# Kernel tuning notes

Measured on AMD Instinct MI355X. Metric: run time of the kernel, lower is better.

Reference implementation:

```python
import jax, jax.numpy as jnp
import numpy as np

B, S_IMG, S_TXT, P, D, HEADS, HD = 1, 2048, 512, 4, 3072, 24, 128


def rmsnorm(x, weight=None, eps=1e-6):
    var = jnp.mean(jnp.square(x), axis=-1, keepdims=True)
    y = x * jax.lax.rsqrt(var + eps)
    return y * weight if weight is not None else y


def apply_rope(x, cos, sin):
    # x: [B,H,S,Dh]; cos/sin: [S,Dh]; interleaved real/imag rotation (diffusers use_real_unbind_dim=-1)
    xr = x.reshape(*x.shape[:-1], -1, 2)
    rot = jnp.stack([-xr[..., 1], xr[..., 0]], axis=-1).reshape(x.shape)
    return x * cos[None, None] + rot * sin[None, None]


def sdpa(q, k, v):
    scores = jnp.einsum('bhqd,bhkd->bhqk', q, k) / jnp.sqrt(jnp.asarray(q.shape[-1], q.dtype))
    return jnp.einsum('bhqk,bhkd->bhqd', jax.nn.softmax(scores, axis=-1), v)


def heads_split(x):
    # [B,S,D] -> [B,H,S,Dh]
    return x.reshape(x.shape[0], x.shape[1], HEADS, HD).transpose(0, 2, 1, 3)


def heads_merge(x):
    # [B,H,S,Dh] -> [B,S,D]
    return x.transpose(0, 2, 1, 3).reshape(x.shape[0], x.shape[2], HEADS * HD)


def setup_inputs() -> dict:
    key = jax.random.key(0)
    ks = jax.random.split(key, 32)
    init = lambda k, shape: (jax.random.normal(k, shape, dtype=jnp.float32) * 0.02)
    inp = {
        'hidden_states': jax.random.normal(ks[0], (B, S_IMG, D), dtype=jnp.float32),
        'encoder_hidden_states': jax.random.normal(ks[1], (B, S_TXT, D), dtype=jnp.float32),
        'ip_encoder_hidden_states': jax.random.normal(ks[2], (B, P, D), dtype=jnp.float32),
        'layer_scale': jax.random.uniform(ks[3], (B,), dtype=jnp.float32),
        'Wq': init(ks[4], (D, D)), 'bq': jnp.zeros((D,), jnp.float32),
        'Wk': init(ks[5], (D, D)), 'bk': jnp.zeros((D,), jnp.float32),
        'Wv': init(ks[6], (D, D)), 'bv': jnp.zeros((D,), jnp.float32),
        'norm_q_w': jnp.ones((HD,), jnp.float32),
        'norm_k_w': jnp.ones((HD,), jnp.float32),
        'Waq': init(ks[7], (D, D)), 'baq': jnp.zeros((D,), jnp.float32),
        'Wak': init(ks[8], (D, D)), 'bak': jnp.zeros((D,), jnp.float32),
        'Wav': init(ks[9], (D, D)), 'bav': jnp.zeros((D,), jnp.float32),
        'norm_aq_w': jnp.ones((HD,), jnp.float32),
        'norm_ak_w': jnp.ones((HD,), jnp.float32),
        'Wk_ip': init(ks[10], (D, D)),
        'Wv_ip': init(ks[11], (D, D)),
        'Wo': init(ks[12], (D, D)), 'bo': jnp.zeros((D,), jnp.float32),
        'Wao': init(ks[13], (D, D)), 'bao': jnp.zeros((D,), jnp.float32),
    }
    # rotary cos/sin over the joint (text+image) sequence, interleaved freqs per diffusers FLUX
    pos = jnp.arange(S_TXT + S_IMG, dtype=jnp.float32)
    inv_freq = 1.0 / (10000.0 ** (jnp.arange(0, HD, 2, dtype=jnp.float32) / HD))
    angles = pos[:, None] * inv_freq[None, :]            # [S, HD/2]
    angles = jnp.repeat(angles, 2, axis=-1)              # [S, HD]
    inp['cos'] = jnp.cos(angles)
    inp['sin'] = jnp.sin(angles)
    return inp


IP_SCALE = 1.0  # self.scale


def reference(hidden_states, encoder_hidden_states, ip_encoder_hidden_states, cos, sin,
              layer_scale, Wq, bq, Wk, bk, Wv, bv, norm_q_w, norm_k_w,
              Waq, baq, Wak, bak, Wav, bav, norm_aq_w, norm_ak_w,
              Wk_ip, Wv_ip, Wo, bo, Wao, bao):
    # image-stream projections
    q = heads_split(hidden_states @ Wq.T + bq)
    k = heads_split(hidden_states @ Wk.T + bk)
    v = heads_split(hidden_states @ Wv.T + bv)
    q = rmsnorm(q, norm_q_w, 1e-6)
    k = rmsnorm(k, norm_k_w, 1e-6)

    # IP-adapter cross-attention (queries = image tokens, kv = IP tokens)
    ip_k = rmsnorm(heads_split(ip_encoder_hidden_states @ Wk_ip.T), None, 1e-5)
    ip_v = heads_split(ip_encoder_hidden_states @ Wv_ip.T)
    ip_out = heads_merge(sdpa(q, ip_k, ip_v))            # [B, S_img, D]

    # text (encoder) stream projections, prepended to joint sequence
    eq = rmsnorm(heads_split(encoder_hidden_states @ Waq.T + baq), norm_aq_w, 1e-6)
    ek = rmsnorm(heads_split(encoder_hidden_states @ Wak.T + bak), norm_ak_w, 1e-6)
    ev = heads_split(encoder_hidden_states @ Wav.T + bav)
    q = jnp.concatenate([eq, q], axis=2)
    k = jnp.concatenate([ek, k], axis=2)
    v = jnp.concatenate([ev, v], axis=2)

    q = apply_rope(q, cos, sin)
    k = apply_rope(k, cos, sin)

    out = heads_merge(sdpa(q, k, v))                     # [B, S_txt+S_img, D]
    n_txt = encoder_hidden_states.shape[1]
    enc_out, img_out = out[:, :n_txt], out[:, n_txt:]

    ls = layer_scale.reshape(-1, 1, 1)
    img_out = img_out + IP_SCALE * ls * ip_out
    img_out = img_out @ Wo.T + bo
    enc_out = enc_out @ Wao.T + bao
    return (img_out, enc_out)
```

## Files before the change

kernel.cpp:

```cpp
#include <hip/hip_runtime.h>

typedef _Float16 half_t;
typedef _Float16 half2v __attribute__((ext_vector_type(2)));
typedef _Float16 half4v __attribute__((ext_vector_type(4)));
typedef _Float16 half8v __attribute__((ext_vector_type(8)));
typedef float    float4v __attribute__((ext_vector_type(4)));
typedef short    short8v __attribute__((ext_vector_type(8)));

#define S_IMG 2048
#define S_TXT 512
#define S_TOT 2560
#define NH    24
#define HD    128
#define DM    3072

__device__ __forceinline__ void gload16(const void* g, void* l) {
  __builtin_amdgcn_global_load_lds(
      (const __attribute__((address_space(1))) unsigned int*)g,
      (__attribute__((address_space(3))) unsigned int*)l, 16, 0, 0);
}

__global__ void cvt_act_kernel(const float* __restrict__ hs, const float* __restrict__ enc,
                               half_t* __restrict__ d) {
  const long NHS = (long)S_IMG * DM;
  const long TOT = NHS + (long)S_TXT * DM;
  long i = ((long)blockIdx.x * 256 + threadIdx.x) * 8;
  long stride = (long)gridDim.x * 256 * 8;
  for (; i < TOT; i += stride) {
    const float* s = i < NHS ? hs + i : enc + (i - NHS);
    float4v v0 = *(const float4v*)(s);
    float4v v1 = *(const float4v*)(s + 4);
    half8v h;
    h[0] = (half_t)v0[0]; h[1] = (half_t)v0[1]; h[2] = (half_t)v0[2]; h[3] = (half_t)v0[3];
    h[4] = (half_t)v1[0]; h[5] = (half_t)v1[1]; h[6] = (half_t)v1[2]; h[7] = (half_t)v1[3];
    *(half8v*)(d + i) = h;
  }
}

__global__ void cvt3_kernel(const float* __restrict__ s0, const float* __restrict__ s1,
                            const float* __restrict__ s2,
                            half_t* __restrict__ d0, half_t* __restrict__ d1,
                            half_t* __restrict__ d2, int n) {
  const float* s = blockIdx.y == 0 ? s0 : (blockIdx.y == 1 ? s1 : s2);
  half_t* d = blockIdx.y == 0 ? d0 : (blockIdx.y == 1 ? d1 : d2);
  int i = (blockIdx.x * 256 + threadIdx.x) * 8;
  int stride = gridDim.x * 256 * 8;
  for (; i < n; i += stride) {
    float4v v0 = *(const float4v*)(s + i);
    float4v v1 = *(const float4v*)(s + i + 4);
    half8v h;
    h[0] = (half_t)v0[0]; h[1] = (half_t)v0[1]; h[2] = (half_t)v0[2]; h[3] = (half_t)v0[3];
    h[4] = (half_t)v1[0]; h[5] = (half_t)v1[1]; h[6] = (half_t)v1[2]; h[7] = (half_t)v1[3];
    *(half8v*)(d + i) = h;
  }
}

template <typename OUT>
__device__ __forceinline__ void gemm_tile(half_t* As, half_t* Bs,
                                          const half_t* __restrict__ A,
                                          const half_t* __restrict__ Bt,
                                          const float* __restrict__ bias,
                                          OUT* __restrict__ C, int bm, int bn) {
  const int K = DM, N = DM;
  const int tid = threadIdx.x, wid = tid >> 6, l = tid & 63;
  const int wm = (wid >> 1) * 64, wn = (wid & 1) * 64;
  const int l15 = l & 15, l4 = l >> 4;
  float4v acc[4][4] = {};

  const int scol = ((l & 3) ^ ((l >> 3) & 3)) * 8;
  const half_t* ga = A + (long)(bm + wid * 32 + (l >> 2)) * K + scol;
  const half_t* gb = Bt + (long)(bn + wid * 32 + (l >> 2)) * K + scol;
  const long rowstep = 16l * K;

#define GSTAGE(T, SEL)                                                        \
  {                                                                           \
    char* a_d = (char*)As + (SEL) * 8192 + wid * 2048;                        \
    char* b_d = (char*)Bs + (SEL) * 8192 + wid * 2048;                        \
    int k0 = (T) * 32;                                                        \
    gload16(ga + k0, a_d);                                                    \
    gload16(ga + rowstep + k0, a_d + 1024);                                   \
    gload16(gb + k0, b_d);                                                    \
    gload16(gb + rowstep + k0, b_d + 1024);                                   \
  }

  GSTAGE(0, 0);
  GSTAGE(1, 1);

  const int NT = K / 32;
  const int cofs = (l4 * 16) ^ (((l15 >> 1) & 3) << 4);
  for (int t = 0; t < NT; t++) {
    int cur = t % 3;
    if (t + 1 < NT) asm volatile("s_waitcnt vmcnt(4)" ::: "memory");
    else            asm volatile("s_waitcnt vmcnt(0)" ::: "memory");
    __builtin_amdgcn_s_barrier();
    __builtin_amdgcn_sched_barrier(0);
    if (t + 2 < NT) GSTAGE(t + 2, (t + 2) % 3);
    __builtin_amdgcn_sched_barrier(0);
    const char* AsB = (const char*)As + cur * 8192;
    const char* BsB = (const char*)Bs + cur * 8192;
    half8v af[4], bf[4];
#pragma unroll
    for (int i = 0; i < 4; i++)
      af[i] = *(const half8v*)(AsB + (wm + i * 16 + l15) * 64 + cofs);
#pragma unroll
    for (int j = 0; j < 4; j++)
      bf[j] = *(const half8v*)(BsB + (wn + j * 16 + l15) * 64 + cofs);
    __builtin_amdgcn_s_setprio(1);
#pragma unroll
    for (int i = 0; i < 4; i++)
#pragma unroll
      for (int j = 0; j < 4; j++)
        acc[i][j] = __builtin_amdgcn_mfma_f32_16x16x32_f16(af[i], bf[j], acc[i][j], 0, 0, 0);
    __builtin_amdgcn_s_setprio(0);
  }
#undef GSTAGE
#pragma unroll
  for (int i = 0; i < 4; i++)
#pragma unroll
    for (int j = 0; j < 4; j++) {
      int row = bm + wm + i * 16 + l4 * 4;
      int col = bn + wn + j * 16 + l15;
      float bv = bias ? bias[col] : 0.0f;
#pragma unroll
      for (int r = 0; r < 4; r++) {
        float v = acc[i][j][r] + bv;
        C[(long)(row + r) * N + col] = (OUT)v;
      }
    }
}

template <int NROW>
__global__ __launch_bounds__(256) void gemm3_kernel(const half_t* __restrict__ A,
                                                    const half_t* __restrict__ W0,
                                                    const half_t* __restrict__ W1,
                                                    const half_t* __restrict__ W2,
                                                    const float* b0, const float* b1, const float* b2,
                                                    half_t* O0, half_t* O1, half_t* O2) {
  __shared__ half_t As[3 * 128 * 32];
  __shared__ half_t Bs[3 * 128 * 32];
  int b = blockIdx.x;
  int q = (72 * NROW) >> 3;
  int wg = (b & 7) * q + (b >> 3);
  int col = wg / NROW, row = wg % NROW;
  int sel = col / 24;
  const half_t* Bt = sel == 0 ? W0 : (sel == 1 ? W1 : W2);
  const float* bias = sel == 0 ? b0 : (sel == 1 ? b1 : b2);
  half_t* C = sel == 0 ? O0 : (sel == 1 ? O1 : O2);
  gemm_tile<half_t>(As, Bs, A, Bt, bias, C, row * 128, (col % 24) * 128);
}

__global__ __launch_bounds__(256) void gemm_out_kernel(const half_t* __restrict__ ocomb,
                                                       const half_t* __restrict__ Wo_h,
                                                       const half_t* __restrict__ Wao_h,
                                                       const float* bo, const float* bao,
                                                       float* out_img, float* out_enc) {
  __shared__ half_t As[3 * 128 * 32];
  __shared__ half_t Bs[3 * 128 * 32];
  int b = blockIdx.x;
  int wg = (b & 7) * 60 + (b >> 3);
  int col = wg / 20, r = wg % 20;
  bool enc = r >= 16;
  const half_t* A = enc ? ocomb : ocomb + (long)S_TXT * DM;
  int bm = (enc ? (r - 16) : r) * 128;
  gemm_tile<float>(As, Bs, A, enc ? Wao_h : Wo_h, enc ? bao : bo,
                   enc ? out_enc : out_img, bm, col * 128);
}

__global__ __launch_bounds__(256) void ip_proj_kernel(const float* __restrict__ x,
                                                      const float* __restrict__ Wk_ip,
                                                      const float* __restrict__ Wv_ip,
                                                      float* __restrict__ outk,
                                                      float* __restrict__ outv) {
  const float* W = blockIdx.y ? Wv_ip : Wk_ip;
  float* out = blockIdx.y ? outv : outk;
  int n = blockIdx.x * 4 + (threadIdx.x >> 6);
  int l = threadIdx.x & 63;
  const float* wr = W + (long)n * DM;
  float acc[4] = {0.f, 0.f, 0.f, 0.f};
  for (int k = l * 4; k < DM; k += 256) {
    float4v wv = *(const float4v*)(wr + k);
#pragma unroll
    for (int p = 0; p < 4; p++) {
      float4v xv = *(const float4v*)(x + p * DM + k);
      acc[p] += wv[0] * xv[0] + wv[1] * xv[1] + wv[2] * xv[2] + wv[3] * xv[3];
    }
  }
#pragma unroll
  for (int off = 32; off; off >>= 1)
#pragma unroll
    for (int p = 0; p < 4; p++) acc[p] += __shfl_xor(acc[p], off, 64);
  if (l == 0)
#pragma unroll
    for (int p = 0; p < 4; p++) out[p * DM + n] = acc[p];
}

__global__ void ip_norm_kernel(const float* __restrict__ kr, const float* __restrict__ vr,
                               half_t* __restrict__ kh, half_t* __restrict__ vh) {
  int t = blockIdx.x;
  int l = threadIdx.x;
  int d = l * 2;
  if (t < 96) {
    int base = (t / 24) * DM + (t % 24) * HD;
    float x0 = kr[base + d], x1 = kr[base + d + 1];
    float ss = x0 * x0 + x1 * x1;
#pragma unroll
    for (int off = 32; off; off >>= 1) ss += __shfl_xor(ss, off, 64);
    float r = rsqrtf(ss * (1.0f / HD) + 1e-5f);
    kh[base + d] = (half_t)(x0 * r);
    kh[base + d + 1] = (half_t)(x1 * r);
  } else {
    int t2 = t - 96;
    int base = (t2 / 24) * DM + (t2 % 24) * HD;
    vh[base + d] = (half_t)vr[base + d];
    vh[base + d + 1] = (half_t)vr[base + d + 1];
  }
}

__global__ __launch_bounds__(256) void prep_kernel(
    const half_t* __restrict__ qraw, const half_t* __restrict__ kraw,
    const half_t* __restrict__ eq, const half_t* __restrict__ ek,
    const float* __restrict__ nqw, const float* __restrict__ nkw,
    const float* __restrict__ naqw, const float* __restrict__ nakw,
    const float* __restrict__ cosb, const float* __restrict__ sinb,
    half_t* __restrict__ qcat, half_t* __restrict__ kcat, half_t* __restrict__ qnr) {
  int task = blockIdx.x * 4 + (threadIdx.x >> 6);
  int l = threadIdx.x & 63;
  int s = task / NH, h = task - (task / NH) * NH;
  int d = l * 2;
  const half_t *qs, *ks;
  const float *wq, *wk;
  if (s < S_TXT) {
    long base = (long)s * DM + h * HD;
    qs = eq + base; ks = ek + base;
    wq = naqw; wk = nakw;
  } else {
    long base = (long)(s - S_TXT) * DM + h * HD;
    qs = qraw + base; ks = kraw + base;
    wq = nqw; wk = nkw;
  }
  half2v qv = *(const half2v*)(qs + d);
  half2v kv = *(const half2v*)(ks + d);
  float q0 = (float)qv[0], q1 = (float)qv[1];
  float k0 = (float)kv[0], k1 = (float)kv[1];
  float ssq = q0 * q0 + q1 * q1;
  float ssk = k0 * k0 + k1 * k1;
#pragma unroll
  for (int off = 32; off; off >>= 1) {
    ssq += __shfl_xor(ssq, off, 64);
    ssk += __shfl_xor(ssk, off, 64);
  }
  float rq = rsqrtf(ssq * (1.0f / HD) + 1e-6f);
  float rk = rsqrtf(ssk * (1.0f / HD) + 1e-6f);
  float qn0 = q0 * rq * wq[d], qn1 = q1 * rq * wq[d + 1];
  float kn0 = k0 * rk * wk[d], kn1 = k1 * rk * wk[d + 1];
  if (s >= S_TXT) {
    half2v o; o[0] = (half_t)qn0; o[1] = (half_t)qn1;
    *(half2v*)(qnr + ((long)h * S_IMG + (s - S_TXT)) * HD + d) = o;
  }
  float c0 = cosb[s * HD + d], c1 = cosb[s * HD + d + 1];
  float s0 = sinb[s * HD + d], s1 = sinb[s * HD + d + 1];
  float qo0 = qn0 * c0 - qn1 * s0, qo1 = qn1 * c1 + qn0 * s1;
  float ko0 = kn0 * c0 - kn1 * s0, ko1 = kn1 * c1 + kn0 * s1;
  long ci = ((long)h * S_TOT + s) * HD + d;
  half2v oq; oq[0] = (half_t)qo0; oq[1] = (half_t)qo1;
  half2v ok; ok[0] = (half_t)ko0; ok[1] = (half_t)ko1;
  *(half2v*)(qcat + ci) = oq;
  *(half2v*)(kcat + ci) = ok;
}

__global__ __launch_bounds__(256) void vtrans_kernel(const half_t* __restrict__ ev,
                                                     const half_t* __restrict__ vraw,
                                                     half_t* __restrict__ vcatT) {
  __shared__ half_t T[64][136];
  int h = blockIdx.y, sb = blockIdx.x * 64;
  int t = threadIdx.x;
#pragma unroll
  for (int i = 0; i < 4; i++) {
    int c = t + i * 256;
    int row = c >> 4, col = (c & 15) * 8;
    int s = sb + row;
    const half_t* src = (s < S_TXT) ? ev + (long)s * DM + h * HD + col
                                    : vraw + (long)(s - S_TXT) * DM + h * HD + col;
    *(half8v*)&T[row][col] = *(const half8v*)src;
  }
  __syncthreads();
#pragma unroll
  for (int i = 0; i < 4; i++) {
    int c = t + i * 256;
    int d = c >> 3, sc = (c & 7) * 8;
    half8v v;
#pragma unroll
    for (int j = 0; j < 8; j++) v[j] = T[sc + j][d];
    *(half8v*)(vcatT + ((long)h * HD + d) * S_TOT + sb + sc) = v;
  }
}

__global__ __launch_bounds__(256) void ip_attn_kernel(const half_t* __restrict__ qnr,
                                                      const half_t* __restrict__ kh,
                                                      const half_t* __restrict__ vh,
                                                      half_t* __restrict__ ipout) {
  int tid = threadIdx.x;
  int task = blockIdx.x * 16 + (tid >> 4);
  int l16 = tid & 15;
  int h = task >> 11;
  int s = task & 2047;
  int d = l16 * 8;
  half8v qv = *(const half8v*)(qnr + ((long)h * S_IMG + s) * HD + d);
  float sc[4];
#pragma unroll
  for (int p = 0; p < 4; p++) {
    half8v kv = *(const half8v*)(kh + p * DM + h * HD + d);
    float a = 0.f;
#pragma unroll
    for (int j = 0; j < 8; j++) a += (float)qv[j] * (float)kv[j];
    sc[p] = a;
  }
#pragma unroll
  for (int off = 8; off; off >>= 1)
#pragma unroll
    for (int p = 0; p < 4; p++) sc[p] += __shfl_xor(sc[p], off, 16);
  float m = fmaxf(fmaxf(sc[0], sc[1]), fmaxf(sc[2], sc[3]));
  float e[4], sum = 0.f;
#pragma unroll
  for (int p = 0; p < 4; p++) { e[p] = __expf((sc[p] - m) * 0.088388347648318447f); sum += e[p]; }
  float inv = 1.0f / sum;
  float o[8] = {};
#pragma unroll
  for (int p = 0; p < 4; p++) {
    half8v vv = *(const half8v*)(vh + p * DM + h * HD + d);
#pragma unroll
    for (int j = 0; j < 8; j++) o[j] += e[p] * (float)vv[j];
  }
  half8v ov;
#pragma unroll
  for (int j = 0; j < 8; j++) ov[j] = (half_t)(o[j] * inv);
  *(half8v*)(ipout + (long)s * DM + h * HD + d) = ov;
}

__global__ __launch_bounds__(256, 2) void flash_kernel(const half_t* __restrict__ qcat,
                                                       const half_t* __restrict__ kcat,
                                                       const half_t* __restrict__ vcatT,
                                                       const half_t* __restrict__ ipout,
                                                       const float* __restrict__ lsp,
                                                       half_t* __restrict__ ocomb) {
  __shared__ half_t Ks[2 * 64 * 128];
  __shared__ half_t Vs[2 * 128 * 64];
  __shared__ half_t Pw[4][16 * 72];
  int b = blockIdx.x;
  int wg = (b & 7) * 60 + (b >> 3);
  const int h = wg / 20, qb = wg % 20;
  const int tid = threadIdx.x, wid = tid >> 6, l = tid & 63;
  const int l15 = l & 15, l4 = l >> 4;
  const float CEXP = 0.12754137969983614f;

  half8v qf[2][4];
#pragma unroll
  for (int t = 0; t < 2; t++) {
    int qrow = qb * 128 + wid * 32 + t * 16 + l15;
    const half_t* qp = qcat + ((long)h * S_TOT + qrow) * HD;
#pragma unroll
    for (int kk = 0; kk < 4; kk++) qf[t][kk] = *(const half8v*)(qp + kk * 32 + l4 * 8);
  }
  float4v o[2][8] = {};
  float lreg[2] = {0.f, 0.f};
  const float ls = lsp[0];

  const char* kb = (const char*)(kcat + (long)h * S_TOT * HD);
  const char* vb = (const char*)(vcatT + (long)h * HD * S_TOT);
  int kof[4];
  long vof[4];
#pragma unroll
  for (int c = 0; c < 4; c++) {
    int L = c * 4096 + tid * 16;
    kof[c] = L ^ (((L >> 8) & 7) << 4);
    int vrow = L >> 7;
    vof[c] = (long)vrow * (S_TOT * 2) + ((L & 127) ^ ((vrow & 7) << 4));
  }

#define STAGE(KT, SEL)                                                        \
  {                                                                           \
    char* kd = (char*)Ks + (SEL) * 16384 + wid * 1024;                        \
    char* vd = (char*)Vs + (SEL) * 16384 + wid * 1024;                        \
    _Pragma("unroll") for (int c = 0; c < 4; c++) {                           \
      gload16(kb + (long)(KT) * 256 + kof[c], kd + c * 4096);                 \
      gload16(vb + vof[c] + (KT) * 2, vd + c * 4096);                         \
    }                                                                         \
  }

  STAGE(0, 0);

  const int NT = S_TOT / 64;
  int sel = 0;
  for (int it = 0; it < NT; it++) {
    asm volatile("s_waitcnt vmcnt(0)" ::: "memory");
    __builtin_amdgcn_s_barrier();
    __builtin_amdgcn_sched_barrier(0);
    if (it + 1 < NT) STAGE((it + 1) * 64, sel ^ 1);

    const char* KsB = (const char*)Ks + sel * 16384;
    const char* VsB = (const char*)Vs + sel * 16384;

    float4v s0[4] = {}, s1[4] = {};
    __builtin_amdgcn_s_setprio(1);
#pragma unroll
    for (int nb = 0; nb < 4; nb++) {
      int krow = nb * 16 + l15;
      int rb = krow << 8;
      int sw = (krow & 7) << 4;
#pragma unroll
      for (int kk = 0; kk < 4; kk++) {
        half8v kf = *(const half8v*)(KsB + rb + ((kk * 64 + l4 * 16) ^ sw));
        s0[nb] = __builtin_amdgcn_mfma_f32_16x16x32_f16(kf, qf[0][kk], s0[nb], 0, 0, 0);
        s1[nb] = __builtin_amdgcn_mfma_f32_16x16x32_f16(kf, qf[1][kk], s1[nb], 0, 0, 0);
      }
    }
    __builtin_amdgcn_s_setprio(0);
#pragma unroll
    for (int t = 0; t < 2; t++) {
      float4v* st = t ? s1 : s0;
      float sum = 0.f;
#pragma unroll
      for (int nb = 0; nb < 4; nb++) {
        half4v ph;
#pragma unroll
        for (int r = 0; r < 4; r++) {
          float e = exp2f(st[nb][r] * CEXP - 2.0f);
          sum += e;
          ph[r] = (half_t)e;
        }
        *(half4v*)&Pw[wid][l15 * 72 + nb * 16 + l4 * 4] = ph;
      }
      sum += __shfl_xor(sum, 16, 64);
      sum += __shfl_xor(sum, 32, 64);
      lreg[t] += sum;
      half8v pa0 = *(const half8v*)&Pw[wid][l15 * 72 + l4 * 8];
      half8v pa1 = *(const half8v*)&Pw[wid][l15 * 72 + 32 + l4 * 8];
      __builtin_amdgcn_s_setprio(1);
#pragma unroll
      for (int cb = 0; cb < 8; cb++) {
        int row = cb * 16 + l15;
        int sw = (row & 7) << 4;
        half8v vf0 = *(const half8v*)(VsB + (row << 7) + ((l4 * 16) ^ sw));
        half8v vf1 = *(const half8v*)(VsB + (row << 7) + ((64 + l4 * 16) ^ sw));
        o[t][cb] = __builtin_amdgcn_mfma_f32_16x16x32_f16(pa0, vf0, o[t][cb], 0, 0, 0);
        o[t][cb] = __builtin_amdgcn_mfma_f32_16x16x32_f16(pa1, vf1, o[t][cb], 0, 0, 0);
      }
      __builtin_amdgcn_s_setprio(0);
    }
    sel ^= 1;
  }
#undef STAGE
#pragma unroll
  for (int t = 0; t < 2; t++) {
    float invq = 1.0f / lreg[t];
#pragma unroll
    for (int r = 0; r < 4; r++) {
      float inv = __shfl(invq, l4 * 4 + r, 64);
      int s = qb * 128 + wid * 32 + t * 16 + l4 * 4 + r;
#pragma unroll
      for (int cb = 0; cb < 8; cb++) {
        int col = h * HD + cb * 16 + l15;
        float val = o[t][cb][r] * inv;
        if (s >= S_TXT) val += ls * (float)ipout[(long)(s - S_TXT) * DM + col];
        ocomb[(long)s * DM + col] = (half_t)val;
      }
    }
  }
}

extern "C" void kernel_launch(void* const* d_in, const int* in_sizes, int n_in,
                              void* d_out, int out_size, void* d_ws, size_t ws_size,
                              hipStream_t stream) {
  (void)in_sizes; (void)n_in; (void)out_size; (void)ws_size;
  const float* hs    = (const float*)d_in[0];
  const float* enc   = (const float*)d_in[1];
  const float* ipenc = (const float*)d_in[2];
  const float* lsc   = (const float*)d_in[3];
  const float* Wq  = (const float*)d_in[4];  const float* bq  = (const float*)d_in[5];
  const float* Wk  = (const float*)d_in[6];  const float* bk  = (const float*)d_in[7];
  const float* Wv  = (const float*)d_in[8];  const float* bv  = (const float*)d_in[9];
  const float* nqw = (const float*)d_in[10]; const float* nkw = (const float*)d_in[11];
  const float* Waq = (const float*)d_in[12]; const float* baq = (const float*)d_in[13];
  const float* Wak = (const float*)d_in[14]; const float* bak = (const float*)d_in[15];
  const float* Wav = (const float*)d_in[16]; const float* bav = (const float*)d_in[17];
  const float* naqw= (const float*)d_in[18]; const float* nakw= (const float*)d_in[19];
  const float* Wkip= (const float*)d_in[20]; const float* Wvip= (const float*)d_in[21];
  const float* Wo  = (const float*)d_in[22]; const float* bo  = (const float*)d_in[23];
  const float* Wao = (const float*)d_in[24]; const float* bao = (const float*)d_in[25];
  const float* cosb= (const float*)d_in[26]; const float* sinb= (const float*)d_in[27];

  const size_t WSZ = (size_t)DM * DM;
  const size_t HSZ = (size_t)S_IMG * DM;
  const size_t ESZ = (size_t)S_TXT * DM;
  const size_t CSZ = (size_t)NH * S_TOT * HD;

  half_t* base = (half_t*)d_ws;
  half_t* W3    = base;
  half_t* hs_h  = W3 + 3 * WSZ;
  half_t* enc_h = hs_h + HSZ;
  half_t* qkvr  = enc_h + ESZ;
  half_t* eqkv  = qkvr + 3 * HSZ;
  half_t* qcat  = eqkv + 3 * ESZ;
  half_t* kcat  = qcat + CSZ;
  half_t* vcatT = kcat + CSZ;

  half_t* q_raw = qkvr;
  half_t* k_raw = qkvr + HSZ;
  half_t* v_raw = qkvr + 2 * HSZ;
  half_t* eq_r  = eqkv;
  half_t* ek_r  = eqkv + ESZ;
  half_t* ev_r  = eqkv + 2 * ESZ;
  half_t* qnr   = hs_h;
  half_t* ipout = qkvr;
  half_t* ocomb = qkvr + HSZ;
  float*  ipk_raw = (float*)enc_h;
  float*  ipv_raw = ipk_raw + 4 * DM;
  half_t* ipk_h  = enc_h + 16 * DM;
  half_t* ipv_h  = ipk_h + 4 * DM;

  cvt_act_kernel<<<2048, 256, 0, stream>>>(hs, enc, hs_h);

  cvt3_kernel<<<dim3(1024, 3), 256, 0, stream>>>(Wq, Wk, Wv, W3, W3 + WSZ, W3 + 2 * WSZ, (int)WSZ);
  gemm3_kernel<16><<<1152, 256, 0, stream>>>(hs_h, W3, W3 + WSZ, W3 + 2 * WSZ,
                                             bq, bk, bv, q_raw, k_raw, v_raw);
  cvt3_kernel<<<dim3(1024, 3), 256, 0, stream>>>(Waq, Wak, Wav, W3, W3 + WSZ, W3 + 2 * WSZ, (int)WSZ);
  gemm3_kernel<4><<<288, 256, 0, stream>>>(enc_h, W3, W3 + WSZ, W3 + 2 * WSZ,
                                           baq, bak, bav, eq_r, ek_r, ev_r);
  ip_proj_kernel<<<dim3(768, 2), 256, 0, stream>>>(ipenc, Wkip, Wvip, ipk_raw, ipv_raw);
  ip_norm_kernel<<<192, 64, 0, stream>>>(ipk_raw, ipv_raw, ipk_h, ipv_h);

  prep_kernel<<<(S_TOT * NH) / 4, 256, 0, stream>>>(q_raw, k_raw, eq_r, ek_r,
                                                    nqw, nkw, naqw, nakw, cosb, sinb,
                                                    qcat, kcat, qnr);
  vtrans_kernel<<<dim3(S_TOT / 64, NH), 256, 0, stream>>>(ev_r, v_raw, vcatT);

  ip_attn_kernel<<<(NH * S_IMG) / 16, 256, 0, stream>>>(qnr, ipk_h, ipv_h, ipout);

  flash_kernel<<<480, 256, 0, stream>>>(qcat, kcat, vcatT, ipout, lsc, ocomb);

  float* out_img = (float*)d_out;
  float* out_enc = (float*)d_out + (size_t)S_IMG * DM;
  cvt3_kernel<<<dim3(1024, 2), 256, 0, stream>>>(Wo, Wao, Wao, W3, W3 + WSZ, W3 + 2 * WSZ, (int)WSZ);
  gemm_out_kernel<<<480, 256, 0, stream>>>(ocomb, W3, W3 + WSZ, bo, bao, out_img, out_enc);
}
```

Measured before the change: 567.9 us.

## Keep softmax probabilities in registers by permuting V key order, defer row-sum reduction

The flash kernel no longer round-trips P through per-wave shared memory. The V-transpose kernel now writes the key dimension in a permuted order so that the MFMA accumulator layout of the score tiles can be fed directly as the A operand of the PV MFMA. The row-sum cross-lane shuffles are moved out of the KV loop and done once at the end, and the PV loop is merged for both query tiles so each V fragment load serves four MFMAs. The cost is a coupled layout contract between the transpose and flash kernels, plus higher register pressure from holding both exponent tiles.

```diff
diff --git a/kernel.cpp b/kernel.cpp
--- a/kernel.cpp
+++ b/kernel.cpp
@@ -291,7 +291,12 @@
     half8v v;
 #pragma unroll
     for (int j = 0; j < 8; j++) v[j] = T[sc + j][d];
-    *(half8v*)(vcatT + ((long)h * HD + d) * S_TOT + sb + sc) = v;
+    int base = (sc & 32) | ((sc & 8) << 1) | ((sc & 16) >> 2);
+    half_t* dst = vcatT + ((long)h * HD + d) * S_TOT + sb;
+    half4v q0; q0[0] = v[0]; q0[1] = v[1]; q0[2] = v[2]; q0[3] = v[3];
+    half4v q1; q1[0] = v[4]; q1[1] = v[5]; q1[2] = v[6]; q1[3] = v[7];
+    *(half4v*)(dst + base) = q0;
+    *(half4v*)(dst + base + 8) = q1;
   }
 }
 
@@ -345,7 +350,6 @@
                                                        half_t* __restrict__ ocomb) {
   __shared__ half_t Ks[2 * 64 * 128];
   __shared__ half_t Vs[2 * 128 * 64];
-  __shared__ half_t Pw[4][16 * 72];
   int b = blockIdx.x;
   int wg = (b & 7) * 60 + (b >> 3);
   const int h = wg / 20, qb = wg % 20;
@@ -362,7 +366,7 @@
     for (int kk = 0; kk < 4; kk++) qf[t][kk] = *(const half8v*)(qp + kk * 32 + l4 * 8);
   }
   float4v o[2][8] = {};
-  float lreg[2] = {0.f, 0.f};
+  float lsum[2] = {0.f, 0.f};
   const float ls = lsp[0];
 
   const char* kb = (const char*)(kcat + (long)h * S_TOT * HD);
@@ -415,41 +419,52 @@
       }
     }
     __builtin_amdgcn_s_setprio(0);
-#pragma unroll
-    for (int t = 0; t < 2; t++) {
-      float4v* st = t ? s1 : s0;
-      float sum = 0.f;
-#pragma unroll
-      for (int nb = 0; nb < 4; nb++) {
-        half4v ph;
+    half8v pa00, pa01, pa10, pa11;
+    {
+      float sum0 = 0.f, sum1 = 0.f;
+      float e0[4][4], e1[4][4];
+#pragma unroll
+      for (int nb = 0; nb < 4; nb++)
 #pragma unroll
         for (int r = 0; r < 4; r++) {
-          float e = exp2f(st[nb][r] * CEXP - 2.0f);
-          sum += e;
-          ph[r] = (half_t)e;
+          float a = exp2f(s0[nb][r] * CEXP - 2.0f);
+          float c = exp2f(s1[nb][r] * CEXP - 2.0f);
+          e0[nb][r] = a; e1[nb][r] = c;
+          sum0 += a; sum1 += c;
         }
-        *(half4v*)&Pw[wid][l15 * 72 + nb * 16 + l4 * 4] = ph;
+      lsum[0] += sum0; lsum[1] += sum1;
+#pragma unroll
+      for (int r = 0; r < 4; r++) {
+        pa00[r] = (half_t)e0[0][r]; pa00[r + 4] = (half_t)e0[1][r];
+        pa01[r] = (half_t)e0[2][r]; pa01[r + 4] = (half_t)e0[3][r];
+        pa10[r] = (half_t)e1[0][r]; pa10[r + 4] = (half_t)e1[1][r];
+        pa11[r] = (half_t)e1[2][r]; pa11[r + 4] = (half_t)e1[3][r];
       }
-      sum += __shfl_xor(sum, 16, 64);
-      sum += __shfl_xor(sum, 32, 64);
-      lreg[t] += sum;
-      half8v pa0 = *(const half8v*)&Pw[wid][l15 * 72 + l4 * 8];
-      half8v pa1 = *(const half8v*)&Pw[wid][l15 * 72 + 32 + l4 * 8];
-      __builtin_amdgcn_s_setprio(1);
-#pragma unroll
-      for (int cb = 0; cb < 8; cb++) {
-        int row = cb * 16 + l15;
-        int sw = (row & 7) << 4;
-        half8v vf0 = *(const half8v*)(VsB + (row << 7) + ((l4 * 16) ^ sw));
-        half8v vf1 = *(const half8v*)(VsB + (row << 7) + ((64 + l4 * 16) ^ sw));
-        o[t][cb] = __builtin_amdgcn_mfma_f32_16x16x32_f16(pa0, vf0, o[t][cb], 0, 0, 0);
-        o[t][cb] = __builtin_amdgcn_mfma_f32_16x16x32_f16(pa1, vf1, o[t][cb], 0, 0, 0);
-      }
-      __builtin_amdgcn_s_setprio(0);
     }
+    __builtin_amdgcn_s_setprio(1);
+#pragma unroll
+    for (int cb = 0; cb < 8; cb++) {
+      int row = cb * 16 + l15;
+      int sw = (row & 7) << 4;
+      half8v vf0 = *(const half8v*)(VsB + (row << 7) + ((l4 * 16) ^ sw));
+      half8v vf1 = *(const half8v*)(VsB + (row << 7) + ((64 + l4 * 16) ^ sw));
+      o[0][cb] = __builtin_amdgcn_mfma_f32_16x16x32_f16(pa00, vf0, o[0][cb], 0, 0, 0);
+      o[0][cb] = __builtin_amdgcn_mfma_f32_16x16x32_f16(pa01, vf1, o[0][cb], 0, 0, 0);
+      o[1][cb] = __builtin_amdgcn_mfma_f32_16x16x32_f16(pa10, vf0, o[1][cb], 0, 0, 0);
+      o[1][cb] = __builtin_amdgcn_mfma_f32_16x16x32_f16(pa11, vf1, o[1][cb], 0, 0, 0);
+    }
+    __builtin_amdgcn_s_setprio(0);
     sel ^= 1;
   }
 #undef STAGE
+  float lreg[2];
+#pragma unroll
+  for (int t = 0; t < 2; t++) {
+    float s = lsum[t];
+    s += __shfl_xor(s, 16, 64);
+    s += __shfl_xor(s, 32, 64);
+    lreg[t] = s;
+  }
 #pragma unroll
   for (int t = 0; t < 2; t++) {
     float invq = 1.0f / lreg[t];
```

Measured after the change: 555.6 us. 1.02x faster.
